# Kernel optimization log

Hardware: AMD Instinct MI355X
Metric: run time of the kernel (lower is better)

The kernel has to match this reference:

```python
import jax, jax.numpy as jnp
import numpy as np

D = 128
HP = 32
WP = 32
M = 64
B = 8
T = 16
DECAY = 2.0
EPS = 1e-5


def _rope(x, h, w):
    # x: (..., D); h, w: integer coords broadcastable against x's leading dims.
    # Replicates the torch in-place update order: the 'second' channel of each
    # pair is rotated using the ALREADY-updated first channel.
    lead = x.shape[:-1]
    d = x.shape[-1]
    xg = x.reshape(lead + (d // 4, 4))
    # channel layout within group g: [4g (h-a), 4g+1 (w-a), 4g+2 (h-b), 4g+3 (w-b)]
    theta = 100.0 ** (-4.0 * jnp.arange(1, d // 4 + 1, dtype=x.dtype) / d)  # (d//4,)
    hf = h[..., None].astype(x.dtype)
    wf = w[..., None].astype(x.dtype)
    ch, sh = jnp.cos(theta * hf), jnp.sin(theta * hf)
    cw, sw = jnp.cos(theta * wf), jnp.sin(theta * wf)
    a, c, b, e = xg[..., 0], xg[..., 1], xg[..., 2], xg[..., 3]
    a2 = a * ch - b * sh
    b2 = b * ch - a2 * sh  # uses updated a2 (in-place semantics)
    c2 = c * cw + e * sw
    e2 = e * cw + c2 * sw  # uses updated c2
    return jnp.stack([a2, c2, b2, e2], axis=-1).reshape(lead + (d,))


def _layernorm(x, g, b):
    mu = jnp.mean(x, axis=-1, keepdims=True)
    var = jnp.mean((x - mu) ** 2, axis=-1, keepdims=True)
    return (x - mu) * jax.lax.rsqrt(var + EPS) * g + b


def setup_inputs() -> dict:
    key = jax.random.key(0)
    ks = jax.random.split(key, 6)
    t = jax.random.normal(ks[0], (B, T, M, D), dtype=jnp.float32)
    mv = jax.random.normal(ks[1], (B, T, HP, WP, D), dtype=jnp.float32)
    positions = jax.random.randint(ks[2], (B, T, M), 0, HP * WP, dtype=jnp.int64)
    Wq = jax.random.normal(ks[3], (D, D), dtype=jnp.float32) * 0.02
    Wk = jax.random.normal(ks[4], (D, D), dtype=jnp.float32) * 0.02
    return {
        "t": t, "mv": mv, "positions": positions,
        "Wq": Wq, "bq": jnp.zeros((D,), jnp.float32),
        "Wk": Wk, "bk": jnp.zeros((D,), jnp.float32),
        "ln_g": jnp.ones((D,), jnp.float32), "ln_b": jnp.zeros((D,), jnp.float32),
    }


def reference(t, mv, positions, Wq, bq, Wk, bk, ln_g, ln_b):
    Bb, Tt, Mm, Dd = t.shape
    _, _, H, W, _ = mv.shape
    P = H * W

    q = t @ Wq.T + bq                     # (B,T,M,D)
    k = mv @ Wk.T + bk                    # (B,T,H,W,D)

    gh, gw = jnp.meshgrid(jnp.arange(H), jnp.arange(W), indexing="ij")
    k = _rope(k, gh, gw)                  # square rope over the patch grid
    ph = positions // W
    pw = positions % W
    q = _rope(q, ph, pw)                  # flat rope at per-token positions

    q = _layernorm(q.reshape(Bb * Tt, Mm, Dd), ln_g, ln_b)
    k = _layernorm(k.reshape(Bb * Tt, P, Dd), ln_g, ln_b)

    att = jnp.einsum("bmd,bpd->bmp", q, k) / jnp.sqrt(jnp.float32(Dd))

    # distance bias
    pos_coords = jnp.stack([ph, pw], axis=-1).astype(jnp.float32)   # (B,T,M,2)
    p = jnp.arange(P)
    patch_coords = jnp.stack([p // W, p % W], axis=-1).astype(jnp.float32)  # (P,2)
    diff = pos_coords[..., None, :] - patch_coords                  # (B,T,M,P,2)
    dist = jnp.sqrt(jnp.sum(diff * diff, axis=-1))
    bias = -dist / (2.0 * DECAY ** 2)
    bias = jnp.where((pos_coords[..., 0] < 0)[..., None], -1e9, bias)
    bias = bias.reshape(Bb * Tt, Mm, P)

    att = jax.nn.softmax(att + bias, axis=-1)
    out = jnp.einsum("bmp,bpd->bmd", att, mv.reshape(Bb * Tt, P, Dd))
    return out.reshape(Bb, Tt, Mm, Dd)
```

## Files before the change

### kernel.cpp

```cpp
#include <hip/hip_runtime.h>
#include <math.h>

#define D   128
#define HP  32
#define WP  32
#define M   64
#define Bb  8
#define Tt  16
#define P   (HP*WP)
#define BT  (Bb*Tt)
#define EPSF 1e-5f
#define SCALE 0.08838834764831845f

typedef __attribute__((ext_vector_type(8))) _Float16 half8;
typedef __attribute__((ext_vector_type(8))) short    short8;
typedef __attribute__((ext_vector_type(4))) float    floatx4;

__global__ __launch_bounds__(1024)
void prep(const float* __restrict__ Wq, const float* __restrict__ Wk,
          _Float16* __restrict__ W16q, _Float16* __restrict__ W16k,
          float2* __restrict__ ropetab)
{
  const int b = blockIdx.x, t = threadIdx.x;
  if (b == 0) {
    const int gq = t >> 5, coord = t & 31;
    const float theta = __powf(100.0f, -4.0f*(float)(gq+1)/128.0f);
    float s, c;
    __sincosf(theta*(float)coord, &s, &c);
    ropetab[t] = make_float2(c, s);
  } else if (b <= 16) {
    const int i = (b-1)*1024 + t;
    W16q[i] = (_Float16)Wq[i];
  } else {
    const int i = (b-17)*1024 + t;
    W16k[i] = (_Float16)Wk[i];
  }
}

__global__ __launch_bounds__(256)
void transpose_v(const float* __restrict__ mv, _Float16* __restrict__ vt)
{
  const int tid = threadIdx.x;
  const int block0 = blockIdx.x * 64;
  __shared__ _Float16 xs[64*128];

  {
    const float4* xg = (const float4*)(mv + (size_t)block0 * D);
    #pragma unroll
    for (int it = 0; it < 4; ++it) {
      const int idx = tid + 256*it;
      const int row = idx >> 4, col8 = idx & 15;
      const float4 f0 = xg[idx*2], f1 = xg[idx*2+1];
      _Float16 h[8] = {(_Float16)f0.x,(_Float16)f0.y,(_Float16)f0.z,(_Float16)f0.w,
                       (_Float16)f1.x,(_Float16)f1.y,(_Float16)f1.z,(_Float16)f1.w};
      const int byte = row*256 + col8*16;
      *(half8*)((char*)xs + (byte ^ ((row&7)<<4))) = *(half8*)h;
    }
  }
  __syncthreads();

  const int bt2 = block0 >> 10;
  const int p0  = block0 & (P-1);
  const int d   = tid & 127, ph = tid >> 7;
  short hv[32];
  #pragma unroll
  for (int i = 0; i < 32; ++i) {
    const int pl = ph*32 + i;
    const int byte = pl*256 + d*2;
    hv[i] = *(const short*)((const char*)xs + (byte ^ ((pl&7)<<4)));
  }
  short8* dst = (short8*)(vt + ((size_t)bt2*D + d)*P + p0 + ph*32);
  #pragma unroll
  for (int i = 0; i < 4; ++i) dst[i] = ((short8*)hv)[i];
}

template<bool IS_Q>
__global__ __launch_bounds__(256)
void proj_reg(const float* __restrict__ xin,
              const _Float16* __restrict__ W16,
              const float* __restrict__ bvec,
              const float* __restrict__ g,
              const float* __restrict__ bln,
              const int*   __restrict__ positions,
              const float2* __restrict__ ropetab,
              _Float16* __restrict__ yout)
{
  const int tid = threadIdx.x;
  const int w = tid >> 6, lane = tid & 63;
  const int gg = lane >> 4, c = lane & 15;
  const int block0 = blockIdx.x * 64;

  __shared__ _Float16 wl[128*128];

  {
    const short8* wg = (const short8*)W16;
    #pragma unroll
    for (int it = 0; it < 8; ++it) {
      const int idx = tid + 256*it;
      const int row = idx >> 4, col8 = idx & 15;
      const short8 v = wg[idx];
      const int byte = row*256 + col8*16;
      *(short8*)((char*)wl + (byte ^ ((row&7)<<4))) = v;
    }
  }
  __syncthreads();

  const float* xr = xin + (size_t)(block0 + w*16 + c) * D;
  half8 aq[4];
  #pragma unroll
  for (int ks = 0; ks < 4; ++ks) {
    const float4 f0 = *(const float4*)(xr + ks*32 + gg*8);
    const float4 f1 = *(const float4*)(xr + ks*32 + gg*8 + 4);
    _Float16 h[8] = {(_Float16)f0.x,(_Float16)f0.y,(_Float16)f0.z,(_Float16)f0.w,
                     (_Float16)f1.x,(_Float16)f1.y,(_Float16)f1.z,(_Float16)f1.w};
    aq[ks] = *(half8*)h;
  }

  floatx4 acc[8];
  #pragma unroll
  for (int jt = 0; jt < 8; ++jt) {
    floatx4 a4 = (floatx4){0.f,0.f,0.f,0.f};
    #pragma unroll
    for (int ks = 0; ks < 4; ++ks) {
      const int brow = jt*16 + c;
      const int byte = brow*256 + (gg*8 + ks*32)*2;
      const half8 bf = *(const half8*)((const char*)wl + (byte ^ ((brow&7)<<4)));
      a4 = __builtin_amdgcn_mfma_f32_16x16x32_f16(aq[ks], bf, a4, 0, 0, 0);
    }
    acc[jt] = a4;
  }

  const int rr = c & 3;
  int coordv[4];
  #pragma unroll
  for (int r = 0; r < 4; ++r) {
    const int grow = block0 + w*16 + gg*4 + r;
    int hh, ww;
    if (IS_Q) { const int pos = positions[grow]; hh = pos >> 5; ww = pos & 31; }
    else      { const int p = grow & (P-1);      hh = p  >> 5; ww = p  & 31; }
    coordv[r] = (rr & 1) ? ww : hh;
  }

  float fin[8][4];
  float s1[4] = {0.f,0.f,0.f,0.f}, s2[4] = {0.f,0.f,0.f,0.f};
  #pragma unroll
  for (int jt = 0; jt < 8; ++jt) {
    const float bj = bvec[jt*16 + c];
    const int gq = jt*4 + (c >> 2);
    #pragma unroll
    for (int r = 0; r < 4; ++r) {
      const float val = acc[jt][r] + bj;
      const float2 tt = ropetab[gq*32 + coordv[r]];
      const float p2 = __shfl_xor(val, 2);
      const float f1v = (rr & 1) ? (val*tt.x + p2*tt.y)
                                 : (val*tt.x - p2*tt.y);
      const float g2 = __shfl_xor(f1v, 2);
      const float fn = (rr >= 2)
          ? ((rr & 1) ? (val*tt.x + g2*tt.y) : (val*tt.x - g2*tt.y))
          : f1v;
      fin[jt][r] = fn;
      s1[r] += fn;
      s2[r] += fn*fn;
    }
  }

  #pragma unroll
  for (int r = 0; r < 4; ++r) {
    #pragma unroll
    for (int off = 1; off <= 8; off <<= 1) {
      s1[r] += __shfl_xor(s1[r], off);
      s2[r] += __shfl_xor(s2[r], off);
    }
  }

  #pragma unroll
  for (int r = 0; r < 4; ++r) {
    const float mu   = s1[r] * (1.f/128.f);
    const float var  = s2[r] * (1.f/128.f) - mu*mu;
    const float rinv = rsqrtf(var + EPSF);
    const int grow = block0 + w*16 + gg*4 + r;
    _Float16* yo = yout + (size_t)grow * D;
    #pragma unroll
    for (int jt = 0; jt < 8; ++jt) {
      const int col = jt*16 + c;
      const float nv = (fin[jt][r] - mu) * rinv * g[col] + bln[col];
      yo[col] = (_Float16)nv;
    }
  }
}

__global__ __launch_bounds__(256)
void attn_mfma(const _Float16* __restrict__ q,
               const _Float16* __restrict__ k,
               const _Float16* __restrict__ vt,
               const int* __restrict__ positions,
               float* __restrict__ out)
{
  const int bt  = blockIdx.x & (BT-1);
  const int qq  = blockIdx.x >> 7;
  const int tid = threadIdx.x;
  const int w   = tid >> 6, lane = tid & 63;
  const int g   = lane >> 4, c = lane & 15;

  __shared__ _Float16 smem_h[4*16*136];
  __shared__ float    l_lds[4][16];
  _Float16 (*pl)[16][88]   = reinterpret_cast<_Float16(*)[16][88]>(smem_h);
  _Float16 (*o16)[16][136] = reinterpret_cast<_Float16(*)[16][136]>(smem_h);

  const _Float16* qrow = q + (size_t)(bt*M + qq*16 + c) * D + g*8;
  half8 aq[4];
  #pragma unroll
  for (int ks = 0; ks < 4; ++ks) aq[ks] = *(const half8*)(qrow + ks*32);

  float ph[4], pw[4];
  #pragma unroll
  for (int r = 0; r < 4; ++r) {
    const int pos = positions[bt*M + qq*16 + g*4 + r];
    ph[r] = (float)(pos >> 5); pw[r] = (float)(pos & 31);
  }

  float lsum[4] = {0.f, 0.f, 0.f, 0.f};
  floatx4 oacc[8];
  #pragma unroll
  for (int dt = 0; dt < 8; ++dt) oacc[dt] = (floatx4){0.f,0.f,0.f,0.f};

  const _Float16* kb = k  + ((size_t)bt * P) * D;
  const _Float16* vb = vt + ((size_t)bt * D) * P;

  for (int t = 0; t < 4; ++t) {
    const int p0 = w*256 + t*64;

    floatx4 s[4];
    #pragma unroll
    for (int pt = 0; pt < 4; ++pt) {
      floatx4 a4 = (floatx4){0.f,0.f,0.f,0.f};
      const _Float16* krow = kb + (size_t)(p0 + pt*16 + c) * D + g*8;
      #pragma unroll
      for (int ks = 0; ks < 4; ++ks)
        a4 = __builtin_amdgcn_mfma_f32_16x16x32_f16(
                 aq[ks], *(const half8*)(krow + ks*32), a4, 0, 0, 0);
      s[pt] = a4;
    }

    #pragma unroll
    for (int pt = 0; pt < 4; ++pt) {
      const int pp = p0 + pt*16 + c;
      const float hh = (float)(pp >> 5), ww = (float)(pp & 31);
      #pragma unroll
      for (int r = 0; r < 4; ++r) {
        const float dx = ph[r] - hh, dy = pw[r] - ww;
        const float sv = s[pt][r]*SCALE - 0.125f*sqrtf(dx*dx + dy*dy);
        const float e  = __expf(sv - 4.0f);
        const _Float16 eh = (_Float16)e;
        pl[w][g*4 + r][pt*16 + c] = eh;
        lsum[r] += (float)eh;
      }
    }

    #pragma unroll
    for (int ks = 0; ks < 2; ++ks) {
      const half8 pa = *(const half8*)(&pl[w][c][ks*32 + g*8]);
      #pragma unroll
      for (int dt = 0; dt < 8; ++dt) {
        const half8 bv = *(const half8*)(vb + (size_t)(dt*16 + c)*P
                                            + p0 + ks*32 + g*8);
        oacc[dt] = __builtin_amdgcn_mfma_f32_16x16x32_f16(pa, bv, oacc[dt], 0,0,0);
      }
    }
  }

  #pragma unroll
  for (int r = 0; r < 4; ++r) {
    #pragma unroll
    for (int off = 1; off <= 8; off <<= 1)
      lsum[r] += __shfl_xor(lsum[r], off);
  }
  if (c == 0) {
    #pragma unroll
    for (int r = 0; r < 4; ++r) l_lds[w][g*4 + r] = lsum[r];
  }

  #pragma unroll
  for (int dt = 0; dt < 8; ++dt)
    #pragma unroll
    for (int r = 0; r < 4; ++r)
      o16[w][g*4 + r][dt*16 + c] = (_Float16)oacc[dt][r];
  __syncthreads();

  const int qi = tid >> 4, dg = tid & 15;
  const float L = l_lds[0][qi] + l_lds[1][qi] + l_lds[2][qi] + l_lds[3][qi];
  const float inv = 1.0f / L;
  float a2[8] = {0.f,0.f,0.f,0.f,0.f,0.f,0.f,0.f};
  #pragma unroll
  for (int w2 = 0; w2 < 4; ++w2) {
    const half8 ov = *(const half8*)(&o16[w2][qi][dg*8]);
    #pragma unroll
    for (int dd = 0; dd < 8; ++dd) a2[dd] += (float)ov[dd];
  }
  float* orow = out + (size_t)(bt*M + qq*16 + qi) * D + dg*8;
  #pragma unroll
  for (int dd = 0; dd < 8; ++dd) orow[dd] = a2[dd] * inv;
}

extern "C" void kernel_launch(void* const* d_in, const int* in_sizes, int n_in,
                              void* d_out, int out_size, void* d_ws, size_t ws_size,
                              hipStream_t stream) {
  const float* t    = (const float*)d_in[0];
  const float* mv   = (const float*)d_in[1];
  const int*   pos  = (const int*)  d_in[2];
  const float* Wq   = (const float*)d_in[3];
  const float* bq   = (const float*)d_in[4];
  const float* Wk   = (const float*)d_in[5];
  const float* bk   = (const float*)d_in[6];
  const float* ln_g = (const float*)d_in[7];
  const float* ln_b = (const float*)d_in[8];
  float* out = (float*)d_out;

  _Float16* qbuf = (_Float16*)d_ws;
  _Float16* kbuf = qbuf + (size_t)BT*M*D;
  _Float16* vtbf = kbuf + (size_t)BT*P*D;
  _Float16* w16q = vtbf + (size_t)BT*P*D;
  _Float16* w16k = w16q + D*D;
  float2*   rtab = (float2*)(w16k + D*D);

  prep<<<33, 1024, 0, stream>>>(Wq, Wk, w16q, w16k, rtab);
  transpose_v<<<BT*P/64, 256, 0, stream>>>(mv, vtbf);
  proj_reg<false><<<BT*P/64, 256, 0, stream>>>(mv, w16k, bk, ln_g, ln_b, nullptr,
                                               rtab, kbuf);
  proj_reg<true ><<<BT*M/64, 256, 0, stream>>>(t,  w16q, bq, ln_g, ln_b, pos,
                                               rtab, qbuf);
  attn_mfma<<<512, 256, 0, stream>>>(qbuf, kbuf, vtbf, pos, out);
}
```

Measured before the change: 102.8 us.

## Split attention over patch halves with merge kernel; fuse V transpose into K projection

The attention kernel now splits the 1024 patches across two blocks per query tile, doubling the grid to 1024 blocks. Each block writes unnormalized partial outputs and row sums to workspace, and a new merge kernel adds the two halves and normalizes. Separately, the V transpose and K projection kernels become one launch whose even blocks do the GEMM and odd blocks do the transpose, so the two independent passes over mv overlap. This trades an extra launch and a round trip of partial outputs through global memory for more parallelism in attention. The pl/o16 shared buffers are no longer aliased, so LDS use per attention block grows.

Result: slower. 111.8 us (+8.8%).

```diff
diff --git a/kernel.cpp b/kernel.cpp
--- a/kernel.cpp
+++ b/kernel.cpp
@@ -37,60 +37,21 @@
   }
 }
 
-__global__ __launch_bounds__(256)
-void transpose_v(const float* __restrict__ mv, _Float16* __restrict__ vt)
-{
-  const int tid = threadIdx.x;
-  const int block0 = blockIdx.x * 64;
-  __shared__ _Float16 xs[64*128];
-
-  {
-    const float4* xg = (const float4*)(mv + (size_t)block0 * D);
-    #pragma unroll
-    for (int it = 0; it < 4; ++it) {
-      const int idx = tid + 256*it;
-      const int row = idx >> 4, col8 = idx & 15;
-      const float4 f0 = xg[idx*2], f1 = xg[idx*2+1];
-      _Float16 h[8] = {(_Float16)f0.x,(_Float16)f0.y,(_Float16)f0.z,(_Float16)f0.w,
-                       (_Float16)f1.x,(_Float16)f1.y,(_Float16)f1.z,(_Float16)f1.w};
-      const int byte = row*256 + col8*16;
-      *(half8*)((char*)xs + (byte ^ ((row&7)<<4))) = *(half8*)h;
-    }
-  }
-  __syncthreads();
-
-  const int bt2 = block0 >> 10;
-  const int p0  = block0 & (P-1);
-  const int d   = tid & 127, ph = tid >> 7;
-  short hv[32];
-  #pragma unroll
-  for (int i = 0; i < 32; ++i) {
-    const int pl = ph*32 + i;
-    const int byte = pl*256 + d*2;
-    hv[i] = *(const short*)((const char*)xs + (byte ^ ((pl&7)<<4)));
-  }
-  short8* dst = (short8*)(vt + ((size_t)bt2*D + d)*P + p0 + ph*32);
-  #pragma unroll
-  for (int i = 0; i < 4; ++i) dst[i] = ((short8*)hv)[i];
-}
-
 template<bool IS_Q>
-__global__ __launch_bounds__(256)
-void proj_reg(const float* __restrict__ xin,
-              const _Float16* __restrict__ W16,
-              const float* __restrict__ bvec,
-              const float* __restrict__ g,
-              const float* __restrict__ bln,
-              const int*   __restrict__ positions,
-              const float2* __restrict__ ropetab,
-              _Float16* __restrict__ yout)
+__device__ __forceinline__
+void gemm_body(const float* __restrict__ xin,
+               const _Float16* __restrict__ W16,
+               const float* __restrict__ bvec,
+               const float* __restrict__ g,
+               const float* __restrict__ bln,
+               const int*   __restrict__ positions,
+               const float2* __restrict__ ropetab,
+               _Float16* __restrict__ yout,
+               _Float16* wl, int block0)
 {
   const int tid = threadIdx.x;
   const int w = tid >> 6, lane = tid & 63;
   const int gg = lane >> 4, c = lane & 15;
-  const int block0 = blockIdx.x * 64;
-
-  __shared__ _Float16 wl[128*128];
 
   {
     const short8* wg = (const short8*)W16;
@@ -189,23 +150,95 @@
   }
 }
 
+__device__ __forceinline__
+void transpose_body(const float* __restrict__ mv, _Float16* __restrict__ vt,
+                    _Float16* xs, int block0)
+{
+  const int tid = threadIdx.x;
+  {
+    const float4* xg = (const float4*)(mv + (size_t)block0 * D);
+    #pragma unroll
+    for (int it = 0; it < 4; ++it) {
+      const int idx = tid + 256*it;
+      const int row = idx >> 4, col8 = idx & 15;
+      const float4 f0 = xg[idx*2], f1 = xg[idx*2+1];
+      _Float16 h[8] = {(_Float16)f0.x,(_Float16)f0.y,(_Float16)f0.z,(_Float16)f0.w,
+                       (_Float16)f1.x,(_Float16)f1.y,(_Float16)f1.z,(_Float16)f1.w};
+      const int byte = row*256 + col8*16;
+      *(half8*)((char*)xs + (byte ^ ((row&7)<<4))) = *(half8*)h;
+    }
+  }
+  __syncthreads();
+
+  const int bt2 = block0 >> 10;
+  const int p0  = block0 & (P-1);
+  const int d   = tid & 127, ph = tid >> 7;
+  short hv[32];
+  #pragma unroll
+  for (int i = 0; i < 32; ++i) {
+    const int pl = ph*32 + i;
+    const int byte = pl*256 + d*2;
+    hv[i] = *(const short*)((const char*)xs + (byte ^ ((pl&7)<<4)));
+  }
+  short8* dst = (short8*)(vt + ((size_t)bt2*D + d)*P + p0 + ph*32);
+  #pragma unroll
+  for (int i = 0; i < 4; ++i) dst[i] = ((short8*)hv)[i];
+}
+
+__global__ __launch_bounds__(256)
+void proj_k_mixed(const float* __restrict__ mv,
+                  const _Float16* __restrict__ w16k,
+                  const float* __restrict__ bk,
+                  const float* __restrict__ g,
+                  const float* __restrict__ bln,
+                  const float2* __restrict__ ropetab,
+                  _Float16* __restrict__ kout,
+                  _Float16* __restrict__ vt)
+{
+  __shared__ _Float16 sm[128*128];
+  const int bx = blockIdx.x;
+  const int tile = bx >> 1;
+  const int block0 = tile * 64;
+  if ((bx & 1) == 0)
+    gemm_body<false>(mv, w16k, bk, g, bln, nullptr, ropetab, kout, sm, block0);
+  else
+    transpose_body(mv, vt, sm, block0);
+}
+
+__global__ __launch_bounds__(256)
+void proj_q(const float* __restrict__ t,
+            const _Float16* __restrict__ w16q,
+            const float* __restrict__ bq,
+            const float* __restrict__ g,
+            const float* __restrict__ bln,
+            const int*   __restrict__ positions,
+            const float2* __restrict__ ropetab,
+            _Float16* __restrict__ qout)
+{
+  __shared__ _Float16 sm[128*128];
+  gemm_body<true>(t, w16q, bq, g, bln, positions, ropetab, qout, sm,
+                  blockIdx.x * 64);
+}
+
 __global__ __launch_bounds__(256)
 void attn_mfma(const _Float16* __restrict__ q,
                const _Float16* __restrict__ k,
                const _Float16* __restrict__ vt,
                const int* __restrict__ positions,
-               float* __restrict__ out)
-{
-  const int bt  = blockIdx.x & (BT-1);
-  const int qq  = blockIdx.x >> 7;
+               float* __restrict__ opart,
+               float* __restrict__ lpart)
+{
+  const int bt   = blockIdx.x & (BT-1);
+  const int rest = blockIdx.x >> 7;
+  const int qq   = rest & 3;
+  const int hf   = rest >> 2;
   const int tid = threadIdx.x;
   const int w   = tid >> 6, lane = tid & 63;
   const int g   = lane >> 4, c = lane & 15;
 
-  __shared__ _Float16 smem_h[4*16*136];
+  __shared__ _Float16 pl[4][16][88];
+  __shared__ _Float16 o16[4][16][136];
   __shared__ float    l_lds[4][16];
-  _Float16 (*pl)[16][88]   = reinterpret_cast<_Float16(*)[16][88]>(smem_h);
-  _Float16 (*o16)[16][136] = reinterpret_cast<_Float16(*)[16][136]>(smem_h);
 
   const _Float16* qrow = q + (size_t)(bt*M + qq*16 + c) * D + g*8;
   half8 aq[4];
@@ -227,8 +260,8 @@
   const _Float16* kb = k  + ((size_t)bt * P) * D;
   const _Float16* vb = vt + ((size_t)bt * D) * P;
 
-  for (int t = 0; t < 4; ++t) {
-    const int p0 = w*256 + t*64;
+  for (int t = 0; t < 2; ++t) {
+    const int p0 = hf*512 + w*128 + t*64;
 
     floatx4 s[4];
     #pragma unroll
@@ -269,6 +302,8 @@
     }
   }
 
+  __syncthreads();
+
   #pragma unroll
   for (int r = 0; r < 4; ++r) {
     #pragma unroll
@@ -288,8 +323,8 @@
   __syncthreads();
 
   const int qi = tid >> 4, dg = tid & 15;
+  const int row = bt*M + qq*16 + qi;
   const float L = l_lds[0][qi] + l_lds[1][qi] + l_lds[2][qi] + l_lds[3][qi];
-  const float inv = 1.0f / L;
   float a2[8] = {0.f,0.f,0.f,0.f,0.f,0.f,0.f,0.f};
   #pragma unroll
   for (int w2 = 0; w2 < 4; ++w2) {
@@ -297,9 +332,27 @@
     #pragma unroll
     for (int dd = 0; dd < 8; ++dd) a2[dd] += (float)ov[dd];
   }
-  float* orow = out + (size_t)(bt*M + qq*16 + qi) * D + dg*8;
-  #pragma unroll
-  for (int dd = 0; dd < 8; ++dd) orow[dd] = a2[dd] * inv;
+  float* orow = opart + (size_t)hf*(BT*M*D) + (size_t)row*D + dg*8;
+  #pragma unroll
+  for (int dd = 0; dd < 8; ++dd) orow[dd] = a2[dd];
+  if (dg == 0) lpart[hf*(BT*M) + row] = L;
+}
+
+__global__ __launch_bounds__(256)
+void attn_merge(const float* __restrict__ opart,
+                const float* __restrict__ lpart,
+                float* __restrict__ out)
+{
+  const int row = blockIdx.x*8 + (threadIdx.x >> 5);
+  const int c4  = (threadIdx.x & 31) * 4;
+  const float L = lpart[row] + lpart[BT*M + row];
+  const float inv = 1.0f / L;
+  const float4 a = *(const float4*)(opart + (size_t)row*D + c4);
+  const float4 b = *(const float4*)(opart + (size_t)(BT*M)*D + (size_t)row*D + c4);
+  float4 o;
+  o.x = (a.x + b.x)*inv; o.y = (a.y + b.y)*inv;
+  o.z = (a.z + b.z)*inv; o.w = (a.w + b.w)*inv;
+  *(float4*)(out + (size_t)row*D + c4) = o;
 }
 
 extern "C" void kernel_launch(void* const* d_in, const int* in_sizes, int n_in,
@@ -322,12 +375,13 @@
   _Float16* w16q = vtbf + (size_t)BT*P*D;
   _Float16* w16k = w16q + D*D;
   float2*   rtab = (float2*)(w16k + D*D);
+  float*    opart = (float*)(rtab + 1024);
+  float*    lpart = opart + 2*(size_t)BT*M*D;
 
   prep<<<33, 1024, 0, stream>>>(Wq, Wk, w16q, w16k, rtab);
-  transpose_v<<<BT*P/64, 256, 0, stream>>>(mv, vtbf);
-  proj_reg<false><<<BT*P/64, 256, 0, stream>>>(mv, w16k, bk, ln_g, ln_b, nullptr,
-                                               rtab, kbuf);
-  proj_reg<true ><<<BT*M/64, 256, 0, stream>>>(t,  w16q, bq, ln_g, ln_b, pos,
-                                               rtab, qbuf);
-  attn_mfma<<<512, 256, 0, stream>>>(qbuf, kbuf, vtbf, pos, out);
-}
+  proj_k_mixed<<<2*BT*P/64, 256, 0, stream>>>(mv, w16k, bk, ln_g, ln_b,
+                                              rtab, kbuf, vtbf);
+  proj_q<<<BT*M/64, 256, 0, stream>>>(t, w16q, bq, ln_g, ln_b, pos, rtab, qbuf);
+  attn_mfma<<<1024, 256, 0, stream>>>(qbuf, kbuf, vtbf, pos, opart, lpart);
+  attn_merge<<<BT*M/8, 256, 0, stream>>>(opart, lpart, out);
+}
```
